# Performance work log

Measured on AMD Instinct MI355X. Metric: run time of the kernel, lower is better.

## Reference

```python
import jax, jax.numpy as jnp
import numpy as np

T, B, NINP, NHID = 256, 64, 512, 512

def _kaiming(key, shape):
    # kaiming_normal_ default: fan_in mode, gain=sqrt(2)
    fan_in = shape[1]
    std = np.sqrt(2.0 / fan_in)
    return jax.random.normal(key, shape, dtype=jnp.float32) * std

def setup_inputs() -> dict:
    key = jax.random.key(0)
    ks = jax.random.split(key, 8)
    return {
        "inputs": jax.random.normal(ks[0], (T, B, NINP), dtype=jnp.float32),
        "sememe_h": jax.random.normal(ks[1], (T, B, NINP), dtype=jnp.float32),
        "hx": jax.random.normal(ks[2], (B, NHID), dtype=jnp.float32),
        "W_ioux": _kaiming(ks[3], (2 * NHID, 2 * NINP)),
        "b_ioux": jnp.zeros((2 * NHID,), dtype=jnp.float32),
        "W_iouh": _kaiming(ks[4], (2 * NHID, NHID)),
        "b_iouh": jnp.zeros((2 * NHID,), dtype=jnp.float32),
        "W_fx": _kaiming(ks[5], (NHID, 2 * NINP)),
        "b_fx": jnp.zeros((NHID,), dtype=jnp.float32),
        "W_Uh": _kaiming(ks[6], (NHID, NHID)),
        "b_Uh": jnp.zeros((NHID,), dtype=jnp.float32),
    }

def reference(inputs, sememe_h, hx, W_ioux, b_ioux, W_iouh, b_iouh, W_fx, b_fx, W_Uh, b_Uh):
    # x: [T, B, 2*ninp] = concat(inputs[t], sememe_h[t])
    x = jnp.concatenate([inputs, sememe_h], axis=-1)
    # Precompute input-side projections for all timesteps (hoisted out of the loop)
    iou_x = jnp.einsum('tbi,gi->tbg', x, W_ioux) + b_ioux   # [T, B, 2*nhid]
    fx_x = jnp.einsum('tbi,hi->tbh', x, W_fx) + b_fx        # [T, B, nhid]

    def step(h, xs):
        ix, fxt = xs
        iou = ix + h @ W_iouh.T + b_iouh
        z, r = jnp.split(iou, 2, axis=1)
        z = jax.nn.sigmoid(z)
        r = jax.nn.sigmoid(r)
        h_tilde = jnp.tanh(fxt + (r * h) @ W_Uh.T + b_Uh)
        h_new = (1.0 - z) * h + z * h_tilde
        return h_new, h_new

    h_last, out = jax.lax.scan(step, hx, (iou_x, fx_x))
    return out, h_last
```

## Files before the change

kernel.cpp:

```cpp
#include <hip/hip_runtime.h>
#include <hip/hip_bf16.h>

typedef _Float16 half4v __attribute__((ext_vector_type(4)));
typedef _Float16 half8v __attribute__((ext_vector_type(8)));
typedef float f32x4 __attribute__((ext_vector_type(4)));

#define T_STEPS 256
#define BATCH 64
#define NHID 512
#define NINP 512
#define MROWS (T_STEPS * BATCH)
#define KDIM (2 * NINP)
#define NOUT (2 * NHID + NHID)


__global__ __launch_bounds__(256) void k_convert_x(
    const float* __restrict__ inp, const float* __restrict__ sem,
    _Float16* __restrict__ xh) {
  int idx = blockIdx.x * 256 + threadIdx.x;
  const int G = MROWS * KDIM / 4;
  for (int g = idx; g < G; g += 2048 * 256) {
    int e = g * 4;
    int m = e >> 10, k = e & 1023;
    const float* src = (k < NINP) ? (inp + (size_t)m * NINP + k)
                                  : (sem + (size_t)m * NINP + (k - NINP));
    float4 v = *(const float4*)src;
    half4v o = { (_Float16)v.x, (_Float16)v.y, (_Float16)v.z, (_Float16)v.w };
    *(half4v*)(xh + (size_t)e) = o;
  }
}

__global__ __launch_bounds__(256) void k_convert_w(
    const float* __restrict__ W_ioux, const float* __restrict__ W_fx,
    const float* __restrict__ b_ioux, const float* __restrict__ b_fx,
    const float* __restrict__ b_iouh, const float* __restrict__ b_Uh,
    _Float16* __restrict__ wbig, float* __restrict__ biasN) {
  int g = blockIdx.x * 256 + threadIdx.x;
  int e = g * 4;
  int n = e >> 10, k = e & 1023;
  const float* src = (n < 2 * NHID) ? (W_ioux + (size_t)n * KDIM + k)
                                    : (W_fx + (size_t)(n - 2 * NHID) * KDIM + k);
  float4 v = *(const float4*)src;
  half4v o = { (_Float16)v.x, (_Float16)v.y, (_Float16)v.z, (_Float16)v.w };
  *(half4v*)(wbig + (size_t)e) = o;
  if (g < NOUT)
    biasN[g] = (g < 2 * NHID) ? (b_ioux[g] + b_iouh[g])
                              : (b_fx[g - 2 * NHID] + b_Uh[g - 2 * NHID]);
}

__global__ __launch_bounds__(256) void k_convert_wrec(
    const float* __restrict__ W_iouh, const float* __restrict__ W_Uh,
    _Float16* __restrict__ wrec) {
  int g = blockIdx.x * 256 + threadIdx.x;
  int e = g * 4;
  const int NI = 2 * NHID * NHID;
  const float* src = (e < NI) ? (W_iouh + e) : (W_Uh + (e - NI));
  float4 v = *(const float4*)src;
  half4v o = { (_Float16)v.x, (_Float16)v.y, (_Float16)v.z, (_Float16)v.w };
  *(half4v*)(wrec + (size_t)e) = o;
}


__device__ __forceinline__ void gload16(const void* g, void* l) {
  __builtin_amdgcn_global_load_lds(
      (const __attribute__((address_space(1))) unsigned int*)g,
      (__attribute__((address_space(3))) unsigned int*)l, 16, 0, 0);
}

__global__ __launch_bounds__(256) void gemm_bt(
    const _Float16* __restrict__ A, const _Float16* __restrict__ Bm,
    const float* __restrict__ biasN, float* __restrict__ C,
    int M, int N, int K) {
  __shared__ __align__(16) _Float16 As[128 * 32];
  __shared__ __align__(16) _Float16 Bs[128 * 32];
  const int tid = threadIdx.x;
  const int lane = tid & 63;
  const int w = tid >> 6;
  const int wr = w >> 1, wc = w & 1;
  const int nbm = M >> 7;
  const int bm = blockIdx.x % nbm, bn = blockIdx.x / nbm;
  const int m0 = bm << 7, n0 = bn << 7;
  const int lr = lane & 15, lh = lane >> 4;

  f32x4 acc[4][4] = {};

  for (int kk = 0; kk < K; kk += 32) {
#pragma unroll
    for (int c = 0; c < 2; ++c) {
      int L = (c * 256 + tid) * 16;
      int row = L >> 6, inrow = L & 63;
      gload16((const char*)A + ((size_t)(m0 + row) * K + kk) * 2 + inrow,
              (char*)As + L);
      gload16((const char*)Bm + ((size_t)(n0 + row) * K + kk) * 2 + inrow,
              (char*)Bs + L);
    }
    __syncthreads();
    half8v af[4], bf[4];
#pragma unroll
    for (int i = 0; i < 4; ++i)
      af[i] = *(const half8v*)&As[(wr * 64 + i * 16 + lr) * 32 + lh * 8];
#pragma unroll
    for (int i = 0; i < 4; ++i)
      bf[i] = *(const half8v*)&Bs[(wc * 64 + i * 16 + lr) * 32 + lh * 8];
#pragma unroll
    for (int i = 0; i < 4; ++i)
#pragma unroll
      for (int j = 0; j < 4; ++j)
        acc[i][j] = __builtin_amdgcn_mfma_f32_16x16x32_f16(af[i], bf[j], acc[i][j], 0, 0, 0);
    __syncthreads();
  }

#pragma unroll
  for (int i = 0; i < 4; ++i)
#pragma unroll
    for (int j = 0; j < 4; ++j) {
      int n = n0 + wc * 64 + j * 16 + lr;
      float bv = biasN[n];
#pragma unroll
      for (int q = 0; q < 4; ++q) {
        int m = m0 + wr * 64 + i * 16 + lh * 4 + q;
        C[(size_t)m * N + n] = acc[i][j][q] + bv;
      }
    }
}


__device__ __forceinline__ float dot8(half8v a, half8v b, float acc) {
  acc = __builtin_amdgcn_fdot2(__builtin_shufflevector(a, a, 0, 1),
                               __builtin_shufflevector(b, b, 0, 1), acc, false);
  acc = __builtin_amdgcn_fdot2(__builtin_shufflevector(a, a, 2, 3),
                               __builtin_shufflevector(b, b, 2, 3), acc, false);
  acc = __builtin_amdgcn_fdot2(__builtin_shufflevector(a, a, 4, 5),
                               __builtin_shufflevector(b, b, 4, 5), acc, false);
  acc = __builtin_amdgcn_fdot2(__builtin_shufflevector(a, a, 6, 7),
                               __builtin_shufflevector(b, b, 6, 7), acc, false);
  return acc;
}

__device__ __forceinline__ float sigm(float v) { return 1.f / (1.f + __expf(-v)); }

__device__ __forceinline__ void wait4(int* f, int need, int lane) {
  int v = need;
  if (lane < 4)
    v = __hip_atomic_load(&f[lane], __ATOMIC_RELAXED, __HIP_MEMORY_SCOPE_AGENT);
  while (__any(v < need)) {
    __builtin_amdgcn_s_sleep(2);
    if (lane < 4)
      v = __hip_atomic_load(&f[lane], __ATOMIC_RELAXED, __HIP_MEMORY_SCOPE_AGENT);
  }
}

__device__ __forceinline__ void st16(unsigned short* p, _Float16 x) {
  __hip_atomic_store(p, __builtin_bit_cast(unsigned short, x),
                     __ATOMIC_RELAXED, __HIP_MEMORY_SCOPE_AGENT);
}

__global__ __launch_bounds__(256, 1) void recur4(
    const _Float16* __restrict__ Wrec, const float* __restrict__ hx,
    const float* __restrict__ proj, unsigned short* __restrict__ hbuf,
    unsigned short* __restrict__ rhbuf, int* __restrict__ flags,
    float* __restrict__ out) {
  __shared__ __align__(16) _Float16 hh[NHID];
  __shared__ __align__(16) _Float16 rr[NHID];
  __shared__ float hout[128];

  const int bid = blockIdx.x;
  const int c = bid & 63, g = bid >> 6;
  const int tid = threadIdx.x;
  const int lane = tid & 63;
  const int w = tid >> 6;
  const int oct = lane >> 3, okt = lane & 7;

  int* hfl = flags + c * 64;
  int* rfl = flags + c * 64 + 8;
  const _Float16* WU = Wrec + (size_t)1024 * 512;
  unsigned short* hbC = hbuf + (size_t)c * 512;
  unsigned short* rbC = rhbuf + (size_t)c * 512;

  float hmy[4] = {0, 0, 0, 0}, zk[4] = {0, 0, 0, 0};
  if (okt == 0) {
#pragma unroll
    for (int p = 0; p < 4; ++p) {
      int u = g * 128 + p * 32 + w * 8 + oct;
      hmy[p] = hx[(size_t)c * 512 + u];
      st16(&hbC[u], (_Float16)hmy[p]);
    }
  }
  __syncthreads();
  if (tid == 0)
    __hip_atomic_store(&hfl[g], 1, __ATOMIC_RELAXED, __HIP_MEMORY_SCOPE_AGENT);

  for (int t = 0; t < T_STEPS; ++t) {
    const float* pb = proj + (size_t)(t * BATCH + c) * NOUT;
    float pzv[4] = {0, 0, 0, 0}, prv[4] = {0, 0, 0, 0}, pfv[4] = {0, 0, 0, 0};
    if (okt == 0) {
#pragma unroll
      for (int p = 0; p < 4; ++p) {
        int k = g * 128 + p * 32 + w * 8 + oct;
        pzv[p] = pb[k];
        prv[p] = pb[512 + k];
        pfv[p] = pb[1024 + k];
      }
    }

    wait4(hfl, t + 1, lane);
    asm volatile("" ::: "memory");
    {
      unsigned v = __hip_atomic_load((const unsigned*)hbC + tid,
                                     __ATOMIC_RELAXED, __HIP_MEMORY_SCOPE_AGENT);
      ((unsigned*)hh)[tid] = v;
    }
    __syncthreads();

#pragma unroll 2
    for (int p = 0; p < 8; ++p) {
      int idx = p * 32 + w * 8 + oct;
      int j = (idx < 128) ? (g * 128 + idx) : (512 + g * 128 + (idx - 128));
      const _Float16* wp = Wrec + (size_t)j * 512 + okt * 8;
      float acc = 0.f;
#pragma unroll
      for (int it = 0; it < 8; ++it) {
        half8v wv = *(const half8v*)(wp + it * 64);
        half8v hv = *(const half8v*)(hh + it * 64 + okt * 8);
        acc = dot8(wv, hv, acc);
      }
      acc += __shfl_xor(acc, 1);
      acc += __shfl_xor(acc, 2);
      acc += __shfl_xor(acc, 4);
      if (okt == 0) {
        if (idx < 128) {
          zk[p] = sigm(acc + pzv[p]);
        } else {
          float rv = sigm(acc + prv[p - 4]);
          st16(&rbC[g * 128 + (idx - 128)], (_Float16)(rv * hmy[p - 4]));
        }
      }
    }
    __syncthreads();
    if (tid == 0)
      __hip_atomic_store(&rfl[g], t + 1, __ATOMIC_RELAXED, __HIP_MEMORY_SCOPE_AGENT);

    wait4(rfl, t + 1, lane);
    asm volatile("" ::: "memory");
    {
      unsigned v = __hip_atomic_load((const unsigned*)rbC + tid,
                                     __ATOMIC_RELAXED, __HIP_MEMORY_SCOPE_AGENT);
      ((unsigned*)rr)[tid] = v;
    }
    __syncthreads();

#pragma unroll 2
    for (int p = 0; p < 4; ++p) {
      int idx = p * 32 + w * 8 + oct;
      int u = g * 128 + idx;
      const _Float16* wp = WU + (size_t)u * 512 + okt * 8;
      float acc = 0.f;
#pragma unroll
      for (int it = 0; it < 8; ++it) {
        half8v wv = *(const half8v*)(wp + it * 64);
        half8v rv = *(const half8v*)(rr + it * 64 + okt * 8);
        acc = dot8(wv, rv, acc);
      }
      acc += __shfl_xor(acc, 1);
      acc += __shfl_xor(acc, 2);
      acc += __shfl_xor(acc, 4);
      if (okt == 0) {
        float v = acc + pfv[p];
        float e = __expf(-2.f * fabsf(v));
        float th = (1.f - e) / (1.f + e);
        th = (v < 0.f) ? -th : th;
        float hn = fmaf(zk[p], th - hmy[p], hmy[p]);
        hmy[p] = hn;
        hout[idx] = hn;
        st16(&hbC[u], (_Float16)hn);
      }
    }
    __syncthreads();
    if (tid == 0)
      __hip_atomic_store(&hfl[g], t + 2, __ATOMIC_RELAXED, __HIP_MEMORY_SCOPE_AGENT);

    if (tid < 128)
      out[(size_t)(t * BATCH + c) * NHID + g * 128 + tid] = hout[tid];
  }

  if (okt == 0) {
#pragma unroll
    for (int p = 0; p < 4; ++p) {
      int u = g * 128 + p * 32 + w * 8 + oct;
      out[(size_t)T_STEPS * BATCH * NHID + (size_t)c * NHID + u] = hmy[p];
    }
  }
}


extern "C" void kernel_launch(void* const* d_in, const int* in_sizes, int n_in,
                              void* d_out, int out_size, void* d_ws, size_t ws_size,
                              hipStream_t stream) {
  const float* inputs = (const float*)d_in[0];
  const float* sememe = (const float*)d_in[1];
  const float* hx     = (const float*)d_in[2];
  const float* W_ioux = (const float*)d_in[3];
  const float* b_ioux = (const float*)d_in[4];
  const float* W_iouh = (const float*)d_in[5];
  const float* b_iouh = (const float*)d_in[6];
  const float* W_fx   = (const float*)d_in[7];
  const float* b_fx   = (const float*)d_in[8];
  const float* W_Uh   = (const float*)d_in[9];
  const float* b_Uh   = (const float*)d_in[10];
  float* out = (float*)d_out;

  char* ws = (char*)d_ws;
  _Float16* xh = (_Float16*)ws;   ws += (size_t)MROWS * KDIM * 2;
  _Float16* wbig = (_Float16*)ws; ws += (size_t)NOUT * KDIM * 2;
  float* biasN = (float*)ws;      ws += (size_t)NOUT * 4;
  _Float16* wrec = (_Float16*)ws; ws += (size_t)(3 * NHID * NHID) * 2;
  float* proj = (float*)ws;       ws += (size_t)MROWS * NOUT * 4;
  unsigned short* hbuf = (unsigned short*)ws;  ws += (size_t)BATCH * NHID * 2;
  unsigned short* rhbuf = (unsigned short*)ws; ws += (size_t)BATCH * NHID * 2;
  int* flags = (int*)ws;          ws += (size_t)BATCH * 64 * 4;

  hipMemsetAsync(flags, 0, (size_t)BATCH * 64 * 4, stream);
  k_convert_x<<<2048, 256, 0, stream>>>(inputs, sememe, xh);
  k_convert_w<<<(NOUT * KDIM / 4) / 256, 256, 0, stream>>>(
      W_ioux, W_fx, b_ioux, b_fx, b_iouh, b_Uh, wbig, biasN);
  k_convert_wrec<<<(3 * NHID * NHID / 4) / 256, 256, 0, stream>>>(W_iouh, W_Uh, wrec);
  gemm_bt<<<(MROWS / 128) * (NOUT / 128), 256, 0, stream>>>(
      xh, wbig, biasN, proj, MROWS, NOUT, KDIM);
  recur4<<<256, 256, 0, stream>>>(wrec, hx, proj, hbuf, rhbuf, flags, out);
}
```

Before: 2.403 ms.

## Restructure recurrence into 16 groups of 16 workgroups with split-K partial sums

```diff
diff --git a/kernel.cpp b/kernel.cpp
--- a/kernel.cpp
+++ b/kernel.cpp
@@ -12,6 +12,11 @@
 #define MROWS (T_STEPS * BATCH)
 #define KDIM (2 * NINP)
 #define NOUT (2 * NHID + NHID)
+
+#define NGRP 16
+#define CPG 4
+#define WPG 16
+#define DPW 32
 
 
 __global__ __launch_bounds__(256) void k_convert_x(
@@ -139,156 +144,176 @@
 
 __device__ __forceinline__ float sigm(float v) { return 1.f / (1.f + __expf(-v)); }
 
-__device__ __forceinline__ void wait4(int* f, int need, int lane) {
+__device__ __forceinline__ void wait16(int* f, int need, int lane) {
   int v = need;
-  if (lane < 4)
+  if (lane < 16)
     v = __hip_atomic_load(&f[lane], __ATOMIC_RELAXED, __HIP_MEMORY_SCOPE_AGENT);
   while (__any(v < need)) {
     __builtin_amdgcn_s_sleep(2);
-    if (lane < 4)
+    if (lane < 16)
       v = __hip_atomic_load(&f[lane], __ATOMIC_RELAXED, __HIP_MEMORY_SCOPE_AGENT);
   }
 }
 
-__device__ __forceinline__ void st16(unsigned short* p, _Float16 x) {
+__device__ __forceinline__ void st16a(unsigned short* p, _Float16 x) {
   __hip_atomic_store(p, __builtin_bit_cast(unsigned short, x),
                      __ATOMIC_RELAXED, __HIP_MEMORY_SCOPE_AGENT);
 }
 
-__global__ __launch_bounds__(256, 1) void recur4(
+__global__ __launch_bounds__(256, 1) void recur6(
     const _Float16* __restrict__ Wrec, const float* __restrict__ hx,
     const float* __restrict__ proj, unsigned short* __restrict__ hbuf,
-    unsigned short* __restrict__ rhbuf, int* __restrict__ flags,
+    float* __restrict__ partials, int* __restrict__ flags,
     float* __restrict__ out) {
-  __shared__ __align__(16) _Float16 hh[NHID];
-  __shared__ __align__(16) _Float16 rr[NHID];
-  __shared__ float hout[128];
+  __shared__ __align__(16) _Float16 hsh[CPG][NHID];
+  __shared__ __align__(16) _Float16 rhsh[CPG][DPW];
+  __shared__ float zsh[CPG][DPW];
+  __shared__ float hfsh[CPG][DPW];
 
   const int bid = blockIdx.x;
-  const int c = bid & 63, g = bid >> 6;
+  const int xcd = bid & 7;
+  const int s = bid >> 3;
+  const int g = s & 15;
+  const int G = ((s >> 4) << 3) + xcd;
   const int tid = threadIdx.x;
   const int lane = tid & 63;
-  const int w = tid >> 6;
-  const int oct = lane >> 3, okt = lane & 7;
-
-  int* hfl = flags + c * 64;
-  int* rfl = flags + c * 64 + 8;
+  const int row8 = tid >> 3, okt = tid & 7;
+  const int i64 = tid >> 2, okt2 = tid & 3;
+
+  int* pfl = flags + G * 32;
+  int* hfl = flags + G * 32 + 16;
   const _Float16* WU = Wrec + (size_t)1024 * 512;
-  unsigned short* hbC = hbuf + (size_t)c * 512;
-  unsigned short* rbC = rhbuf + (size_t)c * 512;
-
-  float hmy[4] = {0, 0, 0, 0}, zk[4] = {0, 0, 0, 0};
-  if (okt == 0) {
-#pragma unroll
-    for (int p = 0; p < 4; ++p) {
-      int u = g * 128 + p * 32 + w * 8 + oct;
-      hmy[p] = hx[(size_t)c * 512 + u];
-      st16(&hbC[u], (_Float16)hmy[p]);
-    }
+  float* pbase = partials + (size_t)G * (WPG * CPG * NHID);
+  unsigned short* hbG = hbuf + (size_t)G * CPG * NHID;
+
+  const int jz = g * DPW + row8;
+  const int jr = 512 + g * DPW + row8;
+
+  if (tid < CPG * DPW) {
+    int c = tid >> 5, d = tid & 31;
+    hfsh[c][d] = hx[(size_t)(G * CPG + c) * NHID + g * DPW + d];
+  }
+  {
+    int base = tid * 8;
+    int c = base >> 9, d = base & 511;
+    float4 v0 = *(const float4*)(hx + (size_t)(G * CPG + c) * NHID + d);
+    float4 v1 = *(const float4*)(hx + (size_t)(G * CPG + c) * NHID + d + 4);
+    half8v o = { (_Float16)v0.x, (_Float16)v0.y, (_Float16)v0.z, (_Float16)v0.w,
+                 (_Float16)v1.x, (_Float16)v1.y, (_Float16)v1.z, (_Float16)v1.w };
+    *(half8v*)&hsh[c][d] = o;
   }
   __syncthreads();
-  if (tid == 0)
-    __hip_atomic_store(&hfl[g], 1, __ATOMIC_RELAXED, __HIP_MEMORY_SCOPE_AGENT);
 
   for (int t = 0; t < T_STEPS; ++t) {
-    const float* pb = proj + (size_t)(t * BATCH + c) * NOUT;
-    float pzv[4] = {0, 0, 0, 0}, prv[4] = {0, 0, 0, 0}, pfv[4] = {0, 0, 0, 0};
+    float pz[CPG], pr[CPG], pf = 0.f;
     if (okt == 0) {
 #pragma unroll
-      for (int p = 0; p < 4; ++p) {
-        int k = g * 128 + p * 32 + w * 8 + oct;
-        pzv[p] = pb[k];
-        prv[p] = pb[512 + k];
-        pfv[p] = pb[1024 + k];
-      }
-    }
-
-    wait4(hfl, t + 1, lane);
+      for (int c = 0; c < CPG; ++c) {
+        const float* pb = proj + (size_t)(t * BATCH + G * CPG + c) * NOUT;
+        pz[c] = pb[jz];
+        pr[c] = pb[g * DPW + row8 + 512];
+      }
+    }
+    if (tid < CPG * DPW) {
+      int c = tid >> 5, d = tid & 31;
+      pf = proj[(size_t)(t * BATCH + G * CPG + c) * NOUT + 1024 + g * DPW + d];
+    }
+
+    if (t > 0) {
+      wait16(hfl, t, lane);
+      asm volatile("" ::: "memory");
+#pragma unroll
+      for (int r = 0; r < 4; ++r) {
+        unsigned v = __hip_atomic_load((const unsigned*)hbG + r * 256 + tid,
+                                       __ATOMIC_RELAXED, __HIP_MEMORY_SCOPE_AGENT);
+        ((unsigned*)hsh)[r * 256 + tid] = v;
+      }
+      __syncthreads();
+    }
+
+    float za[CPG] = {}, ra[CPG] = {};
+#pragma unroll
+    for (int it = 0; it < 8; ++it) {
+      half8v wzv = *(const half8v*)(Wrec + (size_t)jz * 512 + it * 64 + okt * 8);
+      half8v wrv = *(const half8v*)(Wrec + (size_t)jr * 512 + it * 64 + okt * 8);
+#pragma unroll
+      for (int c = 0; c < CPG; ++c) {
+        half8v hv = *(const half8v*)&hsh[c][it * 64 + okt * 8];
+        za[c] = dot8(wzv, hv, za[c]);
+        ra[c] = dot8(wrv, hv, ra[c]);
+      }
+    }
+#pragma unroll
+    for (int c = 0; c < CPG; ++c) {
+      za[c] += __shfl_xor(za[c], 1); za[c] += __shfl_xor(za[c], 2); za[c] += __shfl_xor(za[c], 4);
+      ra[c] += __shfl_xor(ra[c], 1); ra[c] += __shfl_xor(ra[c], 2); ra[c] += __shfl_xor(ra[c], 4);
+    }
+    if (okt == 0) {
+#pragma unroll
+      for (int c = 0; c < CPG; ++c) {
+        zsh[c][row8] = sigm(za[c] + pz[c]);
+        float rv = sigm(ra[c] + pr[c]);
+        rhsh[c][row8] = (_Float16)(rv * hfsh[c][row8]);
+      }
+    }
+    __syncthreads();
+
+    half8v rv[CPG];
+#pragma unroll
+    for (int c = 0; c < CPG; ++c)
+      rv[c] = *(const half8v*)&rhsh[c][okt2 * 8];
+#pragma unroll
+    for (int q = 0; q < 8; ++q) {
+      int i = q * 64 + i64;
+      half8v wv = *(const half8v*)(WU + (size_t)i * 512 + g * DPW + okt2 * 8);
+      float pa[CPG];
+#pragma unroll
+      for (int c = 0; c < CPG; ++c) {
+        float a = dot8(wv, rv[c], 0.f);
+        a += __shfl_xor(a, 1);
+        a += __shfl_xor(a, 2);
+        pa[c] = a;
+      }
+      if (okt2 == 0) {
+#pragma unroll
+        for (int c = 0; c < CPG; ++c)
+          __hip_atomic_store(&pbase[(size_t)(g * CPG + c) * NHID + i], pa[c],
+                             __ATOMIC_RELAXED, __HIP_MEMORY_SCOPE_AGENT);
+      }
+    }
+    __syncthreads();
+    if (tid == 0)
+      __hip_atomic_store(&pfl[g], t + 1, __ATOMIC_RELAXED, __HIP_MEMORY_SCOPE_AGENT);
+
+    wait16(pfl, t + 1, lane);
     asm volatile("" ::: "memory");
-    {
-      unsigned v = __hip_atomic_load((const unsigned*)hbC + tid,
-                                     __ATOMIC_RELAXED, __HIP_MEMORY_SCOPE_AGENT);
-      ((unsigned*)hh)[tid] = v;
-    }
-    __syncthreads();
-
-#pragma unroll 2
-    for (int p = 0; p < 8; ++p) {
-      int idx = p * 32 + w * 8 + oct;
-      int j = (idx < 128) ? (g * 128 + idx) : (512 + g * 128 + (idx - 128));
-      const _Float16* wp = Wrec + (size_t)j * 512 + okt * 8;
-      float acc = 0.f;
-#pragma unroll
-      for (int it = 0; it < 8; ++it) {
-        half8v wv = *(const half8v*)(wp + it * 64);
-        half8v hv = *(const half8v*)(hh + it * 64 + okt * 8);
-        acc = dot8(wv, hv, acc);
-      }
-      acc += __shfl_xor(acc, 1);
-      acc += __shfl_xor(acc, 2);
-      acc += __shfl_xor(acc, 4);
-      if (okt == 0) {
-        if (idx < 128) {
-          zk[p] = sigm(acc + pzv[p]);
-        } else {
-          float rv = sigm(acc + prv[p - 4]);
-          st16(&rbC[g * 128 + (idx - 128)], (_Float16)(rv * hmy[p - 4]));
-        }
-      }
+    if (tid < CPG * DPW) {
+      int c = tid >> 5, d = tid & 31;
+      int u = g * DPW + d;
+      float s2 = 0.f;
+#pragma unroll
+      for (int p = 0; p < WPG; ++p)
+        s2 += __hip_atomic_load(&pbase[(size_t)(p * CPG + c) * NHID + u],
+                                __ATOMIC_RELAXED, __HIP_MEMORY_SCOPE_AGENT);
+      float v = s2 + pf;
+      float e = __expf(-2.f * fabsf(v));
+      float th = (1.f - e) / (1.f + e);
+      th = (v < 0.f) ? -th : th;
+      float hold = hfsh[c][d];
+      float hn = fmaf(zsh[c][d], th - hold, hold);
+      hfsh[c][d] = hn;
+      st16a(&hbG[(size_t)c * NHID + u], (_Float16)hn);
+      out[(size_t)(t * BATCH + G * CPG + c) * NHID + u] = hn;
     }
     __syncthreads();
     if (tid == 0)
-      __hip_atomic_store(&rfl[g], t + 1, __ATOMIC_RELAXED, __HIP_MEMORY_SCOPE_AGENT);
-
-    wait4(rfl, t + 1, lane);
-    asm volatile("" ::: "memory");
-    {
-      unsigned v = __hip_atomic_load((const unsigned*)rbC + tid,
-                                     __ATOMIC_RELAXED, __HIP_MEMORY_SCOPE_AGENT);
-      ((unsigned*)rr)[tid] = v;
-    }
-    __syncthreads();
-
-#pragma unroll 2
-    for (int p = 0; p < 4; ++p) {
-      int idx = p * 32 + w * 8 + oct;
-      int u = g * 128 + idx;
-      const _Float16* wp = WU + (size_t)u * 512 + okt * 8;
-      float acc = 0.f;
-#pragma unroll
-      for (int it = 0; it < 8; ++it) {
-        half8v wv = *(const half8v*)(wp + it * 64);
-        half8v rv = *(const half8v*)(rr + it * 64 + okt * 8);
-        acc = dot8(wv, rv, acc);
-      }
-      acc += __shfl_xor(acc, 1);
-      acc += __shfl_xor(acc, 2);
-      acc += __shfl_xor(acc, 4);
-      if (okt == 0) {
-        float v = acc + pfv[p];
-        float e = __expf(-2.f * fabsf(v));
-        float th = (1.f - e) / (1.f + e);
-        th = (v < 0.f) ? -th : th;
-        float hn = fmaf(zk[p], th - hmy[p], hmy[p]);
-        hmy[p] = hn;
-        hout[idx] = hn;
-        st16(&hbC[u], (_Float16)hn);
-      }
-    }
-    __syncthreads();
-    if (tid == 0)
-      __hip_atomic_store(&hfl[g], t + 2, __ATOMIC_RELAXED, __HIP_MEMORY_SCOPE_AGENT);
-
-    if (tid < 128)
-      out[(size_t)(t * BATCH + c) * NHID + g * 128 + tid] = hout[tid];
-  }
-
-  if (okt == 0) {
-#pragma unroll
-    for (int p = 0; p < 4; ++p) {
-      int u = g * 128 + p * 32 + w * 8 + oct;
-      out[(size_t)T_STEPS * BATCH * NHID + (size_t)c * NHID + u] = hmy[p];
-    }
+      __hip_atomic_store(&hfl[g], t + 1, __ATOMIC_RELAXED, __HIP_MEMORY_SCOPE_AGENT);
+  }
+
+  if (tid < CPG * DPW) {
+    int c = tid >> 5, d = tid & 31;
+    out[(size_t)T_STEPS * BATCH * NHID + (size_t)(G * CPG + c) * NHID + g * DPW + d] =
+        hfsh[c][d];
   }
 }
 
@@ -315,16 +340,16 @@
   float* biasN = (float*)ws;      ws += (size_t)NOUT * 4;
   _Float16* wrec = (_Float16*)ws; ws += (size_t)(3 * NHID * NHID) * 2;
   float* proj = (float*)ws;       ws += (size_t)MROWS * NOUT * 4;
-  unsigned short* hbuf = (unsigned short*)ws;  ws += (size_t)BATCH * NHID * 2;
-  unsigned short* rhbuf = (unsigned short*)ws; ws += (size_t)BATCH * NHID * 2;
-  int* flags = (int*)ws;          ws += (size_t)BATCH * 64 * 4;
-
-  hipMemsetAsync(flags, 0, (size_t)BATCH * 64 * 4, stream);
+  unsigned short* hbuf = (unsigned short*)ws; ws += (size_t)BATCH * NHID * 2;
+  float* partials = (float*)ws;   ws += (size_t)NGRP * WPG * CPG * NHID * 4;
+  int* flags = (int*)ws;          ws += (size_t)NGRP * 32 * 4;
+
+  hipMemsetAsync(flags, 0, (size_t)NGRP * 32 * 4, stream);
   k_convert_x<<<2048, 256, 0, stream>>>(inputs, sememe, xh);
   k_convert_w<<<(NOUT * KDIM / 4) / 256, 256, 0, stream>>>(
       W_ioux, W_fx, b_ioux, b_fx, b_iouh, b_Uh, wbig, biasN);
   k_convert_wrec<<<(3 * NHID * NHID / 4) / 256, 256, 0, stream>>>(W_iouh, W_Uh, wrec);
   gemm_bt<<<(MROWS / 128) * (NOUT / 128), 256, 0, stream>>>(
       xh, wbig, biasN, proj, MROWS, NOUT, KDIM);
-  recur4<<<256, 256, 0, stream>>>(wrec, hx, proj, hbuf, rhbuf, flags, out);
-}
+  recur6<<<NGRP * WPG, 256, 0, stream>>>(wrec, hx, proj, hbuf, partials, flags, out);
+}
```

Result: slower. 2.928 ms (+21.8%).

## Repartition recurrent kernel into per-XCD groups of 8 batches across 32 blocks

Applied to the files above, without the earlier changes.

```diff
diff --git a/kernel.cpp b/kernel.cpp
--- a/kernel.cpp
+++ b/kernel.cpp
@@ -12,6 +12,11 @@
 #define MROWS (T_STEPS * BATCH)
 #define KDIM (2 * NINP)
 #define NOUT (2 * NHID + NHID)
+
+#define NX 8
+#define CPX 8
+#define WPX 32
+#define DPW 16
 
 
 __global__ __launch_bounds__(256) void k_convert_x(
@@ -139,156 +144,185 @@
 
 __device__ __forceinline__ float sigm(float v) { return 1.f / (1.f + __expf(-v)); }
 
-__device__ __forceinline__ void wait4(int* f, int need, int lane) {
+__device__ __forceinline__ void wait32(int* f, int need, int lane) {
   int v = need;
-  if (lane < 4)
-    v = __hip_atomic_load(&f[lane], __ATOMIC_RELAXED, __HIP_MEMORY_SCOPE_AGENT);
+  if (lane < 32)
+    v = __hip_atomic_load(&f[lane * 4], __ATOMIC_RELAXED, __HIP_MEMORY_SCOPE_AGENT);
   while (__any(v < need)) {
-    __builtin_amdgcn_s_sleep(2);
-    if (lane < 4)
-      v = __hip_atomic_load(&f[lane], __ATOMIC_RELAXED, __HIP_MEMORY_SCOPE_AGENT);
-  }
-}
-
-__device__ __forceinline__ void st16(unsigned short* p, _Float16 x) {
+    __builtin_amdgcn_s_sleep(1);
+    if (lane < 32)
+      v = __hip_atomic_load(&f[lane * 4], __ATOMIC_RELAXED, __HIP_MEMORY_SCOPE_AGENT);
+  }
+}
+
+__device__ __forceinline__ void st16a(unsigned short* p, _Float16 x) {
   __hip_atomic_store(p, __builtin_bit_cast(unsigned short, x),
                      __ATOMIC_RELAXED, __HIP_MEMORY_SCOPE_AGENT);
 }
 
-__global__ __launch_bounds__(256, 1) void recur4(
+__global__ __launch_bounds__(256, 1) void recur7(
     const _Float16* __restrict__ Wrec, const float* __restrict__ hx,
     const float* __restrict__ proj, unsigned short* __restrict__ hbuf,
     unsigned short* __restrict__ rhbuf, int* __restrict__ flags,
     float* __restrict__ out) {
-  __shared__ __align__(16) _Float16 hh[NHID];
-  __shared__ __align__(16) _Float16 rr[NHID];
-  __shared__ float hout[128];
+  __shared__ __align__(16) _Float16 hsh[CPX][NHID];
+  __shared__ __align__(16) _Float16 rhsh[CPX][NHID];
+  __shared__ float zsh[CPX][DPW];
+  __shared__ float hfsh[CPX][DPW];
+  __shared__ float houts[CPX][DPW];
 
   const int bid = blockIdx.x;
-  const int c = bid & 63, g = bid >> 6;
+  const int xcd = bid & 7;
+  const int g = bid >> 3;
   const int tid = threadIdx.x;
   const int lane = tid & 63;
   const int w = tid >> 6;
-  const int oct = lane >> 3, okt = lane & 7;
-
-  int* hfl = flags + c * 64;
-  int* rfl = flags + c * 64 + 8;
+  const int cb = xcd * CPX;
+
+  const int idx1 = tid >> 3, okt = tid & 7;
+  const bool isz = idx1 < 16;
+  const int dj = isz ? (g * DPW + idx1) : (512 + g * DPW + (idx1 - 16));
+  const int idx2 = tid >> 4, kix = tid & 15;
+
+  int* rhfl = flags + xcd * 256;
+  int* hfl  = flags + xcd * 256 + 128;
   const _Float16* WU = Wrec + (size_t)1024 * 512;
-  unsigned short* hbC = hbuf + (size_t)c * 512;
-  unsigned short* rbC = rhbuf + (size_t)c * 512;
-
-  float hmy[4] = {0, 0, 0, 0}, zk[4] = {0, 0, 0, 0};
-  if (okt == 0) {
-#pragma unroll
-    for (int p = 0; p < 4; ++p) {
-      int u = g * 128 + p * 32 + w * 8 + oct;
-      hmy[p] = hx[(size_t)c * 512 + u];
-      st16(&hbC[u], (_Float16)hmy[p]);
-    }
+  unsigned short* hbX = hbuf + (size_t)xcd * CPX * NHID;
+  unsigned short* rbX = rhbuf + (size_t)xcd * CPX * NHID;
+
+  if (tid < CPX * DPW) {
+    int c = tid >> 4, d = tid & 15;
+    hfsh[c][d] = hx[(size_t)(cb + c) * NHID + g * DPW + d];
+  }
+#pragma unroll
+  for (int r = 0; r < 16; ++r) {
+    int i2 = r * 256 + tid;
+    int c = i2 >> 9, d = i2 & 511;
+    hsh[c][d] = (_Float16)hx[(size_t)(cb + c) * NHID + d];
   }
   __syncthreads();
-  if (tid == 0)
-    __hip_atomic_store(&hfl[g], 1, __ATOMIC_RELAXED, __HIP_MEMORY_SCOPE_AGENT);
 
   for (int t = 0; t < T_STEPS; ++t) {
-    const float* pb = proj + (size_t)(t * BATCH + c) * NOUT;
-    float pzv[4] = {0, 0, 0, 0}, prv[4] = {0, 0, 0, 0}, pfv[4] = {0, 0, 0, 0};
+    const float* pt = proj + (size_t)(t * BATCH + cb) * NOUT;
+
+    float pzr[CPX], pf[CPX];
     if (okt == 0) {
 #pragma unroll
-      for (int p = 0; p < 4; ++p) {
-        int k = g * 128 + p * 32 + w * 8 + oct;
-        pzv[p] = pb[k];
-        prv[p] = pb[512 + k];
-        pfv[p] = pb[1024 + k];
-      }
-    }
-
-    wait4(hfl, t + 1, lane);
+      for (int c = 0; c < CPX; ++c) pzr[c] = pt[(size_t)c * NOUT + dj];
+    }
+    if (kix == 0) {
+#pragma unroll
+      for (int c = 0; c < CPX; ++c)
+        pf[c] = pt[(size_t)c * NOUT + 1024 + g * DPW + idx2];
+    }
+
+    if (t > 0) {
+      if (w == 0) wait32(hfl, t, lane);
+      __syncthreads();
+      asm volatile("" ::: "memory");
+#pragma unroll
+      for (int r = 0; r < 8; ++r) {
+        int i2 = r * 256 + tid;
+        unsigned v = __hip_atomic_load((const unsigned*)hbX + i2,
+                                       __ATOMIC_RELAXED, __HIP_MEMORY_SCOPE_AGENT);
+        ((unsigned*)hsh)[i2] = v;
+      }
+      __syncthreads();
+    }
+
+    float za[CPX] = {};
+    const _Float16* wrow = Wrec + (size_t)dj * 512 + okt * 8;
+#pragma unroll
+    for (int j = 0; j < 8; ++j) {
+      half8v wv = *(const half8v*)(wrow + j * 64);
+#pragma unroll
+      for (int c = 0; c < CPX; ++c) {
+        half8v hv = *(const half8v*)&hsh[c][j * 64 + okt * 8];
+        za[c] = dot8(wv, hv, za[c]);
+      }
+    }
+#pragma unroll
+    for (int c = 0; c < CPX; ++c) {
+      za[c] += __shfl_xor(za[c], 1);
+      za[c] += __shfl_xor(za[c], 2);
+      za[c] += __shfl_xor(za[c], 4);
+    }
+    if (okt == 0) {
+      if (isz) {
+#pragma unroll
+        for (int c = 0; c < CPX; ++c) zsh[c][idx1] = sigm(za[c] + pzr[c]);
+      } else {
+        int d = idx1 - 16;
+#pragma unroll
+        for (int c = 0; c < CPX; ++c) {
+          float rv = sigm(za[c] + pzr[c]);
+          st16a(&rbX[(size_t)c * NHID + g * DPW + d],
+                (_Float16)(rv * hfsh[c][d]));
+        }
+      }
+    }
+    __syncthreads();
+    if (tid == 0)
+      __hip_atomic_store(&rhfl[g * 4], t + 1, __ATOMIC_RELAXED, __HIP_MEMORY_SCOPE_AGENT);
+
+    if (w == 0) wait32(rhfl, t + 1, lane);
+    __syncthreads();
     asm volatile("" ::: "memory");
-    {
-      unsigned v = __hip_atomic_load((const unsigned*)hbC + tid,
+#pragma unroll
+    for (int r = 0; r < 8; ++r) {
+      int i2 = r * 256 + tid;
+      unsigned v = __hip_atomic_load((const unsigned*)rbX + i2,
                                      __ATOMIC_RELAXED, __HIP_MEMORY_SCOPE_AGENT);
-      ((unsigned*)hh)[tid] = v;
-    }
-    __syncthreads();
-
-#pragma unroll 2
-    for (int p = 0; p < 8; ++p) {
-      int idx = p * 32 + w * 8 + oct;
-      int j = (idx < 128) ? (g * 128 + idx) : (512 + g * 128 + (idx - 128));
-      const _Float16* wp = Wrec + (size_t)j * 512 + okt * 8;
-      float acc = 0.f;
-#pragma unroll
-      for (int it = 0; it < 8; ++it) {
-        half8v wv = *(const half8v*)(wp + it * 64);
-        half8v hv = *(const half8v*)(hh + it * 64 + okt * 8);
-        acc = dot8(wv, hv, acc);
-      }
-      acc += __shfl_xor(acc, 1);
-      acc += __shfl_xor(acc, 2);
-      acc += __shfl_xor(acc, 4);
-      if (okt == 0) {
-        if (idx < 128) {
-          zk[p] = sigm(acc + pzv[p]);
-        } else {
-          float rv = sigm(acc + prv[p - 4]);
-          st16(&rbC[g * 128 + (idx - 128)], (_Float16)(rv * hmy[p - 4]));
-        }
-      }
-    }
-    __syncthreads();
-    if (tid == 0)
-      __hip_atomic_store(&rfl[g], t + 1, __ATOMIC_RELAXED, __HIP_MEMORY_SCOPE_AGENT);
-
-    wait4(rfl, t + 1, lane);
-    asm volatile("" ::: "memory");
-    {
-      unsigned v = __hip_atomic_load((const unsigned*)rbC + tid,
-                                     __ATOMIC_RELAXED, __HIP_MEMORY_SCOPE_AGENT);
-      ((unsigned*)rr)[tid] = v;
-    }
-    __syncthreads();
-
-#pragma unroll 2
-    for (int p = 0; p < 4; ++p) {
-      int idx = p * 32 + w * 8 + oct;
-      int u = g * 128 + idx;
-      const _Float16* wp = WU + (size_t)u * 512 + okt * 8;
-      float acc = 0.f;
-#pragma unroll
-      for (int it = 0; it < 8; ++it) {
-        half8v wv = *(const half8v*)(wp + it * 64);
-        half8v rv = *(const half8v*)(rr + it * 64 + okt * 8);
-        acc = dot8(wv, rv, acc);
-      }
-      acc += __shfl_xor(acc, 1);
-      acc += __shfl_xor(acc, 2);
-      acc += __shfl_xor(acc, 4);
-      if (okt == 0) {
-        float v = acc + pfv[p];
+      ((unsigned*)rhsh)[i2] = v;
+    }
+    __syncthreads();
+
+    float ua[CPX] = {};
+    const _Float16* wurow = WU + (size_t)(g * DPW + idx2) * 512 + kix * 8;
+#pragma unroll
+    for (int j = 0; j < 4; ++j) {
+      half8v wv = *(const half8v*)(wurow + j * 128);
+#pragma unroll
+      for (int c = 0; c < CPX; ++c) {
+        half8v rv2 = *(const half8v*)&rhsh[c][j * 128 + kix * 8];
+        ua[c] = dot8(wv, rv2, ua[c]);
+      }
+    }
+#pragma unroll
+    for (int c = 0; c < CPX; ++c) {
+      ua[c] += __shfl_xor(ua[c], 1);
+      ua[c] += __shfl_xor(ua[c], 2);
+      ua[c] += __shfl_xor(ua[c], 4);
+      ua[c] += __shfl_xor(ua[c], 8);
+    }
+    if (kix == 0) {
+#pragma unroll
+      for (int c = 0; c < CPX; ++c) {
+        float v = ua[c] + pf[c];
         float e = __expf(-2.f * fabsf(v));
         float th = (1.f - e) / (1.f + e);
         th = (v < 0.f) ? -th : th;
-        float hn = fmaf(zk[p], th - hmy[p], hmy[p]);
-        hmy[p] = hn;
-        hout[idx] = hn;
-        st16(&hbC[u], (_Float16)hn);
+        float hold = hfsh[c][idx2];
+        float hn = fmaf(zsh[c][idx2], th - hold, hold);
+        hfsh[c][idx2] = hn;
+        houts[c][idx2] = hn;
+        st16a(&hbX[(size_t)c * NHID + g * DPW + idx2], (_Float16)hn);
       }
     }
     __syncthreads();
     if (tid == 0)
-      __hip_atomic_store(&hfl[g], t + 2, __ATOMIC_RELAXED, __HIP_MEMORY_SCOPE_AGENT);
-
-    if (tid < 128)
-      out[(size_t)(t * BATCH + c) * NHID + g * 128 + tid] = hout[tid];
-  }
-
-  if (okt == 0) {
-#pragma unroll
-    for (int p = 0; p < 4; ++p) {
-      int u = g * 128 + p * 32 + w * 8 + oct;
-      out[(size_t)T_STEPS * BATCH * NHID + (size_t)c * NHID + u] = hmy[p];
-    }
+      __hip_atomic_store(&hfl[g * 4], t + 1, __ATOMIC_RELAXED, __HIP_MEMORY_SCOPE_AGENT);
+
+    if (tid < CPX * DPW) {
+      int c = tid >> 4, d = tid & 15;
+      out[(size_t)(t * BATCH + cb + c) * NHID + g * DPW + d] = houts[c][d];
+    }
+  }
+
+  if (tid < CPX * DPW) {
+    int c = tid >> 4, d = tid & 15;
+    out[(size_t)T_STEPS * BATCH * NHID + (size_t)(cb + c) * NHID + g * DPW + d] =
+        hfsh[c][d];
   }
 }
 
@@ -317,14 +351,14 @@
   float* proj = (float*)ws;       ws += (size_t)MROWS * NOUT * 4;
   unsigned short* hbuf = (unsigned short*)ws;  ws += (size_t)BATCH * NHID * 2;
   unsigned short* rhbuf = (unsigned short*)ws; ws += (size_t)BATCH * NHID * 2;
-  int* flags = (int*)ws;          ws += (size_t)BATCH * 64 * 4;
-
-  hipMemsetAsync(flags, 0, (size_t)BATCH * 64 * 4, stream);
+  int* flags = (int*)ws;          ws += (size_t)NX * 256 * 4;
+
+  hipMemsetAsync(flags, 0, (size_t)NX * 256 * 4, stream);
   k_convert_x<<<2048, 256, 0, stream>>>(inputs, sememe, xh);
   k_convert_w<<<(NOUT * KDIM / 4) / 256, 256, 0, stream>>>(
       W_ioux, W_fx, b_ioux, b_fx, b_iouh, b_Uh, wbig, biasN);
   k_convert_wrec<<<(3 * NHID * NHID / 4) / 256, 256, 0, stream>>>(W_iouh, W_Uh, wrec);
   gemm_bt<<<(MROWS / 128) * (NOUT / 128), 256, 0, stream>>>(
       xh, wbig, biasN, proj, MROWS, NOUT, KDIM);
-  recur4<<<256, 256, 0, stream>>>(wrec, hx, proj, hbuf, rhbuf, flags, out);
-}
+  recur7<<<NX * WPX, 256, 0, stream>>>(wrec, hx, proj, hbuf, rhbuf, flags, out);
+}
```

New measurement: 3.857 ms. 1.61x slower.
